# Optimization experiments

Hardware: AMD Instinct MI355X
Metric: run time of the kernel (lower is better)

The kernel has to match this reference:

```python
import jax, jax.numpy as jnp
import numpy as np

N_NODES = 100000
N_EDGES = 1600000
IN_CH = 256
OUT_CH = 128
EPS = 1e-12


def setup_inputs() -> dict:
    key = jax.random.key(0)
    k1, k2, k3 = jax.random.split(key, 3)
    x = jax.random.normal(k1, (N_NODES, IN_CH), dtype=jnp.float32)
    edge_index = jax.random.randint(k2, (2, N_EDGES), 0, N_NODES, dtype=jnp.int64)
    W = jax.random.normal(k3, (IN_CH, OUT_CH), dtype=jnp.float32) / np.float32(np.sqrt(IN_CH))
    b = jnp.zeros((OUT_CH,), dtype=jnp.float32)
    return {"x": x, "edge_index": edge_index, "W": W, "b": b}


def reference(x, edge_index, W, b):
    n = x.shape[0]
    # GCNConv: linear transform first, then normalized aggregation with self-loops
    h = x @ W  # [N, out]
    loops = jnp.arange(n, dtype=edge_index.dtype)
    row = jnp.concatenate([edge_index[0], loops])  # source nodes
    col = jnp.concatenate([edge_index[1], loops])  # destination nodes
    deg = jax.ops.segment_sum(jnp.ones_like(col, dtype=h.dtype), col, num_segments=n)
    dinv = jnp.where(deg > 0, jax.lax.rsqrt(jnp.maximum(deg, 1.0)), 0.0)  # deg^-1/2, inf->0
    wgt = dinv[row] * dinv[col]  # symmetric normalization per edge
    agg = jax.ops.segment_sum(h[row] * wgt[:, None], col, num_segments=n) + b  # [N, out]
    # min-max scale per node (dim=1)
    zmin = agg.min(axis=1, keepdims=True)
    zmax = agg.max(axis=1, keepdims=True)
    z = (agg - zmin) / (zmax - zmin)
    # F.normalize: L2 along dim=1 with eps clamp
    nrm = jnp.maximum(jnp.linalg.norm(z, axis=1, keepdims=True), EPS)
    return z / nrm
```

## Files before the change

kernel.cpp:

```cpp
#include <hip/hip_runtime.h>
#include <hip/hip_bf16.h>

#define N_NODES 100000
#define N_EDGES 1600000
#define IN_CH 256
#define OUT_CH 128

#define BSZ 512
#define NBUCK 196
#define BCAP 9216
#define CSC 8192

#define GEMM_ROWS 32

typedef __attribute__((ext_vector_type(8))) short short8;
typedef __attribute__((ext_vector_type(4))) float floatx4;
typedef __attribute__((ext_vector_type(2))) float float2v;

union bfu { __hip_bfloat16 b; unsigned short u; };

__device__ inline unsigned short f2bf(float v) {
    bfu cv; cv.b = __float2bfloat16(v); return cv.u;
}
__device__ inline float bf2f(unsigned short u) {
    bfu cv; cv.u = u; return __bfloat162float(cv.b);
}

__device__ inline void pkacc(float2v& acc, unsigned g) {
    float2v v;
    v.x = __uint_as_float(g << 16);
    v.y = __uint_as_float(g & 0xffff0000u);
    asm("v_pk_add_f32 %0, %1, %2" : "=v"(acc) : "v"(v), "v"(acc));
}

__global__ __launch_bounds__(256) void pa_scatter(const int* __restrict__ rows,
                                                  const int* __restrict__ cols,
                                                  int* __restrict__ bcursor,
                                                  unsigned* __restrict__ ebuf) {
    __shared__ int lcnt[NBUCK];
    __shared__ int lbase[NBUCK];
    int t = threadIdx.x;
    if (t < NBUCK) lcnt[t] = 0;
    __syncthreads();
    int s0 = blockIdx.x * CSC;
    int e1 = min(N_EDGES, s0 + CSC);
    for (int i = s0 + t; i < e1; i += 256) atomicAdd(&lcnt[cols[i] >> 9], 1);
    __syncthreads();
    if (t < NBUCK) {
        int c = lcnt[t];
        lbase[t] = c ? atomicAdd(&bcursor[t], c) : 0;
        lcnt[t] = 0;
    }
    __syncthreads();
    for (int i = s0 + t; i < e1; i += 256) {
        int c = cols[i], r = rows[i];
        int bk = c >> 9;
        int rank = atomicAdd(&lcnt[bk], 1);
        ebuf[bk * BCAP + lbase[bk] + rank] = ((unsigned)(c & (BSZ - 1)) << 17) | (unsigned)r;
    }
}

__global__ __launch_bounds__(256) void pb_build(const unsigned* __restrict__ ebuf,
                                                const int* __restrict__ bcursor,
                                                int* __restrict__ cnt,
                                                int* __restrict__ base,
                                                float* __restrict__ dinv,
                                                int* __restrict__ es) {
    __shared__ int nh[BSZ];
    __shared__ int sc[BSZ];
    __shared__ int lcur[BSZ];
    int t = threadIdx.x;
    int bk = blockIdx.x;
    int bb = bk * BCAP;
    int bc = bcursor[bk];
    nh[t] = 0; nh[t + 256] = 0;
    lcur[t] = 0; lcur[t + 256] = 0;
    __syncthreads();
    for (int i = t; i < bc; i += 256) atomicAdd(&nh[ebuf[bb + i] >> 17], 1);
    __syncthreads();
    sc[t] = nh[t]; sc[t + 256] = nh[t + 256];
    __syncthreads();
    for (int off = 1; off < BSZ; off <<= 1) {
        int v0 = (t >= off) ? sc[t - off] : 0;
        int i1 = t + 256;
        int v1 = (i1 >= off) ? sc[i1 - off] : 0;
        __syncthreads();
        sc[t] += v0; sc[i1] += v1;
        __syncthreads();
    }
#pragma unroll
    for (int q = 0; q < 2; ++q) {
        int dl = t + q * 256;
        int node = bk * BSZ + dl;
        if (node < N_NODES) {
            int c = nh[dl];
            cnt[node] = c;
            base[node] = bb + sc[dl] - c;
            dinv[node] = rsqrtf((float)(c + 1));
        }
    }
    for (int i = t; i < bc; i += 256) {
        unsigned v = ebuf[bb + i];
        int dl = v >> 17;
        int src = (int)(v & 0x1FFFFu);
        int rank = atomicAdd(&lcur[dl], 1);
        es[bb + sc[dl] - nh[dl] + rank] = src << 8;
    }
}

__global__ void k_prep_w(const float* __restrict__ W,
                         unsigned short* __restrict__ wb_hi,
                         unsigned short* __restrict__ wb_lo) {
    int t = blockIdx.x * 256 + threadIdx.x;
    if (t >= IN_CH * OUT_CH) return;
    int j = t & 7;
    int lane = (t >> 3) & 63;
    int s = (t >> 9) & 7;
    int nt = t >> 12;
    int k = s * 32 + (lane >> 4) * 8 + j;
    int n = nt * 16 + (lane & 15);
    float w = W[k * OUT_CH + n];
    unsigned short hi = f2bf(w);
    wb_hi[t] = hi;
    wb_lo[t] = f2bf(w - bf2f(hi));
}

__global__ __launch_bounds__(512) void k_gemm(const float* __restrict__ x,
                                              const unsigned short* __restrict__ wb_hi,
                                              const unsigned short* __restrict__ wb_lo,
                                              const float* __restrict__ dinv,
                                              unsigned short* __restrict__ hbs) {
    __shared__ short8 xbh[1024];
    __shared__ short8 xbl[1024];
    int t = threadIdx.x;
    int wv = t >> 6;
    int lane = t & 63;
    int row0 = blockIdx.x * GEMM_ROWS;

    short8 Bh[8], Bl[8];
    const short8* bhp = (const short8*)wb_hi + (size_t)wv * 8 * 64 + lane;
    const short8* blp = (const short8*)wb_lo + (size_t)wv * 8 * 64 + lane;
#pragma unroll
    for (int s = 0; s < 8; ++s) {
        Bh[s] = bhp[s * 64];
        Bl[s] = blp[s * 64];
    }

#pragma unroll
    for (int q = 0; q < 2; ++q) {
        int slot = q * 512 + t;
        int ms = slot >> 9;
        int s  = (slot >> 6) & 7;
        int l  = slot & 63;
        int row = row0 + ms * 16 + (l & 15);
        int col = s * 32 + (l >> 4) * 8;
        const float4* xp = (const float4*)(x + (size_t)row * IN_CH + col);
        float4 v0 = xp[0];
        float4 v1 = xp[1];
        float xv[8] = {v0.x, v0.y, v0.z, v0.w, v1.x, v1.y, v1.z, v1.w};
        short8 hh, ll;
#pragma unroll
        for (int j = 0; j < 8; ++j) {
            unsigned short hi = f2bf(xv[j]);
            hh[j] = (short)hi;
            ll[j] = (short)f2bf(xv[j] - bf2f(hi));
        }
        xbh[slot] = hh;
        xbl[slot] = ll;
    }
    __syncthreads();

    int r15 = lane & 15;
    int quad = lane >> 4;

    floatx4 acc[2];
#pragma unroll
    for (int ms = 0; ms < 2; ++ms) {
        acc[ms] = (floatx4){0.f, 0.f, 0.f, 0.f};
#pragma unroll
        for (int s = 0; s < 8; ++s) {
            short8 ah = xbh[(ms * 8 + s) * 64 + lane];
            short8 al = xbl[(ms * 8 + s) * 64 + lane];
            acc[ms] = __builtin_amdgcn_mfma_f32_16x16x32_bf16(ah, Bh[s], acc[ms], 0, 0, 0);
            acc[ms] = __builtin_amdgcn_mfma_f32_16x16x32_bf16(ah, Bl[s], acc[ms], 0, 0, 0);
            acc[ms] = __builtin_amdgcn_mfma_f32_16x16x32_bf16(al, Bh[s], acc[ms], 0, 0, 0);
        }
    }

#pragma unroll
    for (int ms = 0; ms < 2; ++ms)
#pragma unroll
        for (int r = 0; r < 4; ++r) {
            int row = row0 + ms * 16 + quad * 4 + r;
            size_t idx = (size_t)row * OUT_CH + wv * 16 + r15;
            hbs[idx] = f2bf(acc[ms][r] * dinv[row]);
        }
}

__global__ __launch_bounds__(256) void k_agg_fin(const unsigned short* __restrict__ hbs,
                                                 const float* __restrict__ dinv,
                                                 const int* __restrict__ es,
                                                 const int* __restrict__ base,
                                                 const int* __restrict__ cnt,
                                                 const float* __restrict__ b,
                                                 float* __restrict__ out) {
    int node = (blockIdx.x * 256 + threadIdx.x) >> 6;
    int lane = threadIdx.x & 63;
    if (node >= N_NODES) return;

    const char* hb = (const char*)hbs;
    float dn = dinv[node];
    float2 bv = ((const float2*)b)[lane];

    int st = __builtin_amdgcn_readfirstlane(base[node]);
    int d  = __builtin_amdgcn_readfirstlane(cnt[node]);

    unsigned gs = *((const unsigned*)(hb + (size_t)node * 256) + lane);
    float2v acc;
    acc.x = __uint_as_float(gs << 16);
    acc.y = __uint_as_float(gs & 0xffff0000u);

    int sid = (lane < d) ? es[st + lane] : 0;
    int dc = d < 64 ? d : 64;

    int j = 0;
    for (; j + 16 <= dc; j += 16) {
        unsigned g[16];
#pragma unroll
        for (int k = 0; k < 16; ++k) {
            int off = __builtin_amdgcn_readlane(sid, j + k);
            g[k] = *((const unsigned*)(hb + (unsigned)off) + lane);
        }
#pragma unroll
        for (int k = 0; k < 16; ++k) pkacc(acc, g[k]);
    }
    if (j + 8 <= dc) {
        unsigned g[8];
#pragma unroll
        for (int k = 0; k < 8; ++k) {
            int off = __builtin_amdgcn_readlane(sid, j + k);
            g[k] = *((const unsigned*)(hb + (unsigned)off) + lane);
        }
#pragma unroll
        for (int k = 0; k < 8; ++k) pkacc(acc, g[k]);
        j += 8;
    }
    if (j + 4 <= dc) {
        unsigned g[4];
#pragma unroll
        for (int k = 0; k < 4; ++k) {
            int off = __builtin_amdgcn_readlane(sid, j + k);
            g[k] = *((const unsigned*)(hb + (unsigned)off) + lane);
        }
#pragma unroll
        for (int k = 0; k < 4; ++k) pkacc(acc, g[k]);
        j += 4;
    }
    for (; j < dc; ++j) {
        int off = __builtin_amdgcn_readlane(sid, j);
        pkacc(acc, *((const unsigned*)(hb + (unsigned)off) + lane));
    }
    for (; j < d; ++j) {
        int off = __builtin_amdgcn_readfirstlane(es[st + j]);
        pkacc(acc, *((const unsigned*)(hb + (unsigned)off) + lane));
    }

    float ax = dn * acc.x + bv.x;
    float ay = dn * acc.y + bv.y;

    float lmin = fminf(ax, ay), lmax = fmaxf(ax, ay);
#pragma unroll
    for (int m = 32; m; m >>= 1) {
        lmin = fminf(lmin, __shfl_xor(lmin, m, 64));
        lmax = fmaxf(lmax, __shfl_xor(lmax, m, 64));
    }
    float scale = 1.0f / (lmax - lmin);
    float zx = (ax - lmin) * scale;
    float zy = (ay - lmin) * scale;
    float ss = zx * zx + zy * zy;
#pragma unroll
    for (int m = 32; m; m >>= 1) ss += __shfl_xor(ss, m, 64);
    float inv = 1.0f / fmaxf(sqrtf(ss), 1e-12f);
    float2 o;
    o.x = zx * inv;
    o.y = zy * inv;
    ((float2*)(out + (size_t)node * OUT_CH))[lane] = o;
}

extern "C" void kernel_launch(void* const* d_in, const int* in_sizes, int n_in,
                              void* d_out, int out_size, void* d_ws, size_t ws_size,
                              hipStream_t stream) {
    const float* x = (const float*)d_in[0];
    const int* ei = (const int*)d_in[1];
    const float* W = (const float*)d_in[2];
    const float* b = (const float*)d_in[3];
    float* out = (float*)d_out;

    char* ws = (char*)d_ws;
    size_t o = 0;
    auto alloc = [&](size_t bytes) { void* p = ws + o; o = (o + bytes + 255) & ~(size_t)255; return p; };
    float* dinv    = (float*)alloc((size_t)N_NODES * 4);
    int*   cnt     = (int*)  alloc((size_t)N_NODES * 4);
    int*   base    = (int*)  alloc((size_t)N_NODES * 4);
    int*   bcursor = (int*)  alloc(NBUCK * 4);
    unsigned short* wb_hi = (unsigned short*)alloc((size_t)IN_CH * OUT_CH * 2);
    unsigned short* wb_lo = (unsigned short*)alloc((size_t)IN_CH * OUT_CH * 2);
    unsigned short* hbs = (unsigned short*)alloc((size_t)N_NODES * OUT_CH * 2);
    unsigned* ebuf = (unsigned*)alloc((size_t)NBUCK * BCAP * 4);
    int*   es      = (int*)  alloc((size_t)NBUCK * BCAP * 4);

    const int* rows = ei;
    const int* cols = ei + N_EDGES;

    hipMemsetAsync(bcursor, 0, NBUCK * sizeof(int), stream);
    pa_scatter<<<(N_EDGES + CSC - 1) / CSC, 256, 0, stream>>>(rows, cols, bcursor, ebuf);
    pb_build<<<NBUCK, 256, 0, stream>>>(ebuf, bcursor, cnt, base, dinv, es);

    k_prep_w<<<(IN_CH * OUT_CH + 255) / 256, 256, 0, stream>>>(W, wb_hi, wb_lo);
    k_gemm<<<N_NODES / GEMM_ROWS, 512, 0, stream>>>(x, wb_hi, wb_lo, dinv, hbs);

    k_agg_fin<<<(N_NODES + 3) / 4, 256, 0, stream>>>(hbs, dinv, es, base, cnt, b, out);
}
```

Baseline: 304.6 us.

## Aggregate four nodes per wavefront with 16-byte gathers and padded zero row

Reworks the aggregation kernel so each wavefront handles four nodes with 16 lanes each, so every lane gathers 16-byte chunks instead of 4-byte words. Neighbor indices are broadcast within each 16-lane group via ds_bpermute, and the loads are software-pipelined in batches of 16 edges. Missing edges are redirected to an extra zeroed row appended to the bf16 feature buffer, so there are no tail branches. The cost is divergence when degrees differ across the four nodes, since every group runs the maximum iteration count.

```diff
diff --git a/kernel.cpp b/kernel.cpp
--- a/kernel.cpp
+++ b/kernel.cpp
@@ -204,87 +204,112 @@
                                                  const int* __restrict__ cnt,
                                                  const float* __restrict__ b,
                                                  float* __restrict__ out) {
-    int node = (blockIdx.x * 256 + threadIdx.x) >> 6;
-    int lane = threadIdx.x & 63;
-    if (node >= N_NODES) return;
+    int t = threadIdx.x;
+    int lane = t & 63;
+    int ll = lane & 15;
+    int node = blockIdx.x * 16 + (t >> 4);
 
     const char* hb = (const char*)hbs;
+    int lane_byte = ll << 4;
+    int bidx = (lane & 48) << 2;
+
     float dn = dinv[node];
-    float2 bv = ((const float2*)b)[lane];
-
-    int st = __builtin_amdgcn_readfirstlane(base[node]);
-    int d  = __builtin_amdgcn_readfirstlane(cnt[node]);
-
-    unsigned gs = *((const unsigned*)(hb + (size_t)node * 256) + lane);
-    float2v acc;
-    acc.x = __uint_as_float(gs << 16);
-    acc.y = __uint_as_float(gs & 0xffff0000u);
-
-    int sid = (lane < d) ? es[st + lane] : 0;
-    int dc = d < 64 ? d : 64;
-
-    int j = 0;
-    for (; j + 16 <= dc; j += 16) {
-        unsigned g[16];
-#pragma unroll
-        for (int k = 0; k < 16; ++k) {
-            int off = __builtin_amdgcn_readlane(sid, j + k);
-            g[k] = *((const unsigned*)(hb + (unsigned)off) + lane);
-        }
-#pragma unroll
-        for (int k = 0; k < 16; ++k) pkacc(acc, g[k]);
-    }
-    if (j + 8 <= dc) {
-        unsigned g[8];
-#pragma unroll
-        for (int k = 0; k < 8; ++k) {
-            int off = __builtin_amdgcn_readlane(sid, j + k);
-            g[k] = *((const unsigned*)(hb + (unsigned)off) + lane);
-        }
-#pragma unroll
-        for (int k = 0; k < 8; ++k) pkacc(acc, g[k]);
-        j += 8;
-    }
-    if (j + 4 <= dc) {
-        unsigned g[4];
-#pragma unroll
-        for (int k = 0; k < 4; ++k) {
-            int off = __builtin_amdgcn_readlane(sid, j + k);
-            g[k] = *((const unsigned*)(hb + (unsigned)off) + lane);
-        }
-#pragma unroll
-        for (int k = 0; k < 4; ++k) pkacc(acc, g[k]);
-        j += 4;
-    }
-    for (; j < dc; ++j) {
-        int off = __builtin_amdgcn_readlane(sid, j);
-        pkacc(acc, *((const unsigned*)(hb + (unsigned)off) + lane));
-    }
-    for (; j < d; ++j) {
-        int off = __builtin_amdgcn_readfirstlane(es[st + j]);
-        pkacc(acc, *((const unsigned*)(hb + (unsigned)off) + lane));
-    }
-
-    float ax = dn * acc.x + bv.x;
-    float ay = dn * acc.y + bv.y;
-
-    float lmin = fminf(ax, ay), lmax = fmaxf(ax, ay);
-#pragma unroll
-    for (int m = 32; m; m >>= 1) {
+    int d  = cnt[node];
+    int st = base[node];
+
+    float4 bv0 = ((const float4*)b)[ll * 2];
+    float4 bv1 = ((const float4*)b)[ll * 2 + 1];
+
+    uint4 gs = *(const uint4*)(hb + ((size_t)node << 8) + lane_byte);
+    float2v acc[4];
+    acc[0].x = __uint_as_float(gs.x << 16); acc[0].y = __uint_as_float(gs.x & 0xffff0000u);
+    acc[1].x = __uint_as_float(gs.y << 16); acc[1].y = __uint_as_float(gs.y & 0xffff0000u);
+    acc[2].x = __uint_as_float(gs.z << 16); acc[2].y = __uint_as_float(gs.z & 0xffff0000u);
+    acc[3].x = __uint_as_float(gs.w << 16); acc[3].y = __uint_as_float(gs.w & 0xffff0000u);
+
+    int dm = d;
+    dm = max(dm, __shfl_xor(dm, 16, 64));
+    dm = max(dm, __shfl_xor(dm, 32, 64));
+    int iters = __builtin_amdgcn_readfirstlane((dm + 15) >> 4);
+
+    const int zoff = N_NODES << 8;
+
+    for (int it = 0; it < iters; ++it) {
+        int jb = it << 4;
+        int off = zoff;
+        if (jb + ll < d) off = es[st + jb + ll];
+
+        uint4 ga[4], gb[4];
+#pragma unroll
+        for (int k = 0; k < 4; ++k) {
+            int ro = __builtin_amdgcn_ds_bpermute(bidx + (k << 2), off);
+            ga[k] = *(const uint4*)(hb + (unsigned)(ro + lane_byte));
+        }
+#pragma unroll
+        for (int k = 0; k < 4; ++k) {
+            int ro = __builtin_amdgcn_ds_bpermute(bidx + ((4 + k) << 2), off);
+            gb[k] = *(const uint4*)(hb + (unsigned)(ro + lane_byte));
+        }
+#pragma unroll
+        for (int k = 0; k < 4; ++k) {
+            pkacc(acc[0], ga[k].x); pkacc(acc[1], ga[k].y);
+            pkacc(acc[2], ga[k].z); pkacc(acc[3], ga[k].w);
+        }
+#pragma unroll
+        for (int k = 0; k < 4; ++k) {
+            int ro = __builtin_amdgcn_ds_bpermute(bidx + ((8 + k) << 2), off);
+            ga[k] = *(const uint4*)(hb + (unsigned)(ro + lane_byte));
+        }
+#pragma unroll
+        for (int k = 0; k < 4; ++k) {
+            pkacc(acc[0], gb[k].x); pkacc(acc[1], gb[k].y);
+            pkacc(acc[2], gb[k].z); pkacc(acc[3], gb[k].w);
+        }
+#pragma unroll
+        for (int k = 0; k < 4; ++k) {
+            int ro = __builtin_amdgcn_ds_bpermute(bidx + ((12 + k) << 2), off);
+            gb[k] = *(const uint4*)(hb + (unsigned)(ro + lane_byte));
+        }
+#pragma unroll
+        for (int k = 0; k < 4; ++k) {
+            pkacc(acc[0], ga[k].x); pkacc(acc[1], ga[k].y);
+            pkacc(acc[2], ga[k].z); pkacc(acc[3], ga[k].w);
+        }
+#pragma unroll
+        for (int k = 0; k < 4; ++k) {
+            pkacc(acc[0], gb[k].x); pkacc(acc[1], gb[k].y);
+            pkacc(acc[2], gb[k].z); pkacc(acc[3], gb[k].w);
+        }
+    }
+
+    float v[8];
+    v[0] = dn * acc[0].x + bv0.x;  v[1] = dn * acc[0].y + bv0.y;
+    v[2] = dn * acc[1].x + bv0.z;  v[3] = dn * acc[1].y + bv0.w;
+    v[4] = dn * acc[2].x + bv1.x;  v[5] = dn * acc[2].y + bv1.y;
+    v[6] = dn * acc[3].x + bv1.z;  v[7] = dn * acc[3].y + bv1.w;
+
+    float lmin = v[0], lmax = v[0];
+#pragma unroll
+    for (int i = 1; i < 8; ++i) { lmin = fminf(lmin, v[i]); lmax = fmaxf(lmax, v[i]); }
+#pragma unroll
+    for (int m = 8; m; m >>= 1) {
         lmin = fminf(lmin, __shfl_xor(lmin, m, 64));
         lmax = fmaxf(lmax, __shfl_xor(lmax, m, 64));
     }
     float scale = 1.0f / (lmax - lmin);
-    float zx = (ax - lmin) * scale;
-    float zy = (ay - lmin) * scale;
-    float ss = zx * zx + zy * zy;
-#pragma unroll
-    for (int m = 32; m; m >>= 1) ss += __shfl_xor(ss, m, 64);
+    float z[8];
+    float ss = 0.f;
+#pragma unroll
+    for (int i = 0; i < 8; ++i) { z[i] = (v[i] - lmin) * scale; ss += z[i] * z[i]; }
+#pragma unroll
+    for (int m = 8; m; m >>= 1) ss += __shfl_xor(ss, m, 64);
     float inv = 1.0f / fmaxf(sqrtf(ss), 1e-12f);
-    float2 o;
-    o.x = zx * inv;
-    o.y = zy * inv;
-    ((float2*)(out + (size_t)node * OUT_CH))[lane] = o;
+
+    float4 o0 = {z[0] * inv, z[1] * inv, z[2] * inv, z[3] * inv};
+    float4 o1 = {z[4] * inv, z[5] * inv, z[6] * inv, z[7] * inv};
+    float4* op = (float4*)(out + (size_t)node * OUT_CH);
+    op[ll * 2] = o0;
+    op[ll * 2 + 1] = o1;
 }
 
 extern "C" void kernel_launch(void* const* d_in, const int* in_sizes, int n_in,
@@ -305,7 +330,7 @@
     int*   bcursor = (int*)  alloc(NBUCK * 4);
     unsigned short* wb_hi = (unsigned short*)alloc((size_t)IN_CH * OUT_CH * 2);
     unsigned short* wb_lo = (unsigned short*)alloc((size_t)IN_CH * OUT_CH * 2);
-    unsigned short* hbs = (unsigned short*)alloc((size_t)N_NODES * OUT_CH * 2);
+    unsigned short* hbs = (unsigned short*)alloc((size_t)(N_NODES + 1) * OUT_CH * 2);
     unsigned* ebuf = (unsigned*)alloc((size_t)NBUCK * BCAP * 4);
     int*   es      = (int*)  alloc((size_t)NBUCK * BCAP * 4);
 
@@ -313,11 +338,12 @@
     const int* cols = ei + N_EDGES;
 
     hipMemsetAsync(bcursor, 0, NBUCK * sizeof(int), stream);
+    hipMemsetAsync(hbs + (size_t)N_NODES * OUT_CH, 0, OUT_CH * 2, stream);
     pa_scatter<<<(N_EDGES + CSC - 1) / CSC, 256, 0, stream>>>(rows, cols, bcursor, ebuf);
     pb_build<<<NBUCK, 256, 0, stream>>>(ebuf, bcursor, cnt, base, dinv, es);
 
     k_prep_w<<<(IN_CH * OUT_CH + 255) / 256, 256, 0, stream>>>(W, wb_hi, wb_lo);
     k_gemm<<<N_NODES / GEMM_ROWS, 512, 0, stream>>>(x, wb_hi, wb_lo, dinv, hbs);
 
-    k_agg_fin<<<(N_NODES + 3) / 4, 256, 0, stream>>>(hbs, dinv, es, base, cnt, b, out);
-}
+    k_agg_fin<<<N_NODES / 16, 256, 0, stream>>>(hbs, dinv, es, base, cnt, b, out);
+}
```

New measurement: 307.4 us. About the same (+0.9%).
